# Optimization experiments

Hardware: AMD Instinct MI355X
Metric: run time of the kernel (lower is better)

The kernel has to match this reference:

```python
import jax, jax.numpy as jnp
import numpy as np

# static multi-scale pyramid (must match spatial_shapes array in setup_inputs)
SPATIAL = ((100, 100), (50, 50), (25, 25), (13, 13))
E, H, L, P = 256, 8, 4, 8   # embed_dims, num_heads, num_levels, num_points
BS, NQ = 2, 10000
LEN_VAL = sum(h * w for h, w in SPATIAL)


def _bilinear_gather(val, grid, Hs, Ws):
    """val: [BH, Hs*Ws, d]; grid: [BH, N, 2] in [-1,1].
    Matches F.grid_sample(mode='bilinear', padding_mode='zeros', align_corners=False)."""
    x = (grid[..., 0] + 1.0) * (Ws * 0.5) - 0.5
    y = (grid[..., 1] + 1.0) * (Hs * 0.5) - 0.5
    x0 = jnp.floor(x).astype(jnp.int32)
    y0 = jnp.floor(y).astype(jnp.int32)
    x1, y1 = x0 + 1, y0 + 1
    wx1 = x - x0.astype(x.dtype)
    wy1 = y - y0.astype(y.dtype)
    wx0, wy0 = 1.0 - wx1, 1.0 - wy1

    def corner(xi, yi, w):
        valid = (xi >= 0) & (xi < Ws) & (yi >= 0) & (yi < Hs)
        idx = jnp.clip(yi, 0, Hs - 1) * Ws + jnp.clip(xi, 0, Ws - 1)  # [BH, N]
        v = jnp.take_along_axis(val, idx[..., None], axis=1)          # [BH, N, d]
        return v * (w * valid.astype(w.dtype))[..., None]

    return (corner(x0, y0, wx0 * wy0) + corner(x1, y0, wx1 * wy0)
            + corner(x0, y1, wx0 * wy1) + corner(x1, y1, wx1 * wy1))


def setup_inputs() -> dict:
    key = jax.random.key(0)
    ks = jax.random.split(key, 10)
    scale = 1.0 / np.sqrt(E)
    inp = {
        'query': jax.random.normal(ks[0], (BS, NQ, E), jnp.float32),
        'value': jax.random.normal(ks[1], (BS, LEN_VAL, E), jnp.float32),
        'query_pos': 0.1 * jax.random.normal(ks[2], (BS, NQ, E), jnp.float32),
        'reference_points': jax.random.uniform(ks[3], (BS, NQ, L, 2), jnp.float32),
        'spatial_shapes': jnp.array(SPATIAL, dtype=jnp.int32),
        'W_off': 0.02 * jax.random.normal(ks[4], (E, H * L * P * 2), jnp.float32),
        'b_off': 0.5 * jax.random.normal(ks[5], (H * L * P * 2,), jnp.float32),
        'W_attn': 0.02 * jax.random.normal(ks[6], (E, H * L * P), jnp.float32),
        'b_attn': jnp.zeros((H * L * P,), jnp.float32),
        'W_val': scale * jax.random.normal(ks[7], (E, E), jnp.float32),
        'b_val': jnp.zeros((E,), jnp.float32),
        'W_out': scale * jax.random.normal(ks[8], (E, E), jnp.float32),
        'b_out': jnp.zeros((E,), jnp.float32),
    }
    return inp


def reference(query, value, query_pos, reference_points, spatial_shapes,
              W_off, b_off, W_attn, b_attn, W_val, b_val, W_out, b_out):
    d = E // H
    q = query + query_pos                                        # [bs, nq, E]
    bs, nq, _ = q.shape
    v = (value @ W_val + b_val).reshape(bs, LEN_VAL, H, d)       # [bs, len, H, d]
    off = (q @ W_off + b_off).reshape(bs, nq, H, L, P, 2)
    aw = jax.nn.softmax((q @ W_attn + b_attn).reshape(bs, nq, H, L * P), axis=-1)
    aw = aw.reshape(bs, nq, H, L, P)
    # normalizer is (W, H) per level
    norm = jnp.stack([spatial_shapes[:, 1], spatial_shapes[:, 0]], -1).astype(q.dtype)
    loc = reference_points[:, :, None, :, None, :] + off / norm[None, None, None, :, None, :]
    grids = 2.0 * loc - 1.0                                      # [bs, nq, H, L, P, 2]

    out = jnp.zeros((bs, nq, H, d), q.dtype)
    start = 0
    for lvl, (Hs, Ws) in enumerate(SPATIAL):
        v_l = v[:, start:start + Hs * Ws]                        # [bs, HW, H, d]
        start += Hs * Ws
        v_l = v_l.transpose(0, 2, 1, 3).reshape(bs * H, Hs * Ws, d)
        g_l = grids[:, :, :, lvl].transpose(0, 2, 1, 3, 4).reshape(bs * H, nq * P, 2)
        s = _bilinear_gather(v_l, g_l, Hs, Ws).reshape(bs, H, nq, P, d)
        w_l = aw[:, :, :, lvl].transpose(0, 2, 1, 3)             # [bs, H, nq, P]
        out = out + jnp.einsum('bhnpc,bhnp->bnhc', s, w_l)
    return out.reshape(bs, nq, E) @ W_out + b_out
```

## Files before the change

kernel.cpp:

```cpp
#include <hip/hip_runtime.h>


#define EE   256
#define HH   8
#define LL   4
#define NQq  10000
#define BSB  2
#define LENV 13294
#define MQ   16
#define ROWS_V (BSB * LENV)

#define VWS_OFF 393216

typedef unsigned short u16;
typedef unsigned int   u32;
typedef __attribute__((ext_vector_type(8))) short bf16x8;
typedef __attribute__((ext_vector_type(4))) float f32x4;

__device__ __forceinline__ u32 bf16_of(float f) {
  u32 u = __float_as_uint(f);
  return (u + 0x7FFFu + ((u >> 16) & 1u)) >> 16;
}
__device__ __forceinline__ float blo(u32 u) { return __uint_as_float(u << 16); }
__device__ __forceinline__ float bhi(u32 u) { return __uint_as_float(u & 0xFFFF0000u); }

__device__ __forceinline__ uint4 pack8(const float* f) {
  uint4 u;
  u.x = bf16_of(f[0]) | (bf16_of(f[1]) << 16);
  u.y = bf16_of(f[2]) | (bf16_of(f[3]) << 16);
  u.z = bf16_of(f[4]) | (bf16_of(f[5]) << 16);
  u.w = bf16_of(f[6]) | (bf16_of(f[7]) << 16);
  return u;
}

__device__ __forceinline__ void acc8(float o[8], uint4 q, float w) {
  o[0] += w * blo(q.x); o[1] += w * bhi(q.x);
  o[2] += w * blo(q.y); o[3] += w * bhi(q.y);
  o[4] += w * blo(q.z); o[5] += w * bhi(q.z);
  o[6] += w * blo(q.w); o[7] += w * bhi(q.w);
}

__global__ __launch_bounds__(64) void k_prep(
    const float* __restrict__ W_off, const float* __restrict__ W_attn,
    const float* __restrict__ W_val, const float* __restrict__ W_out,
    u16* __restrict__ wcat, u16* __restrict__ wval, u16* __restrict__ wout) {
  const int tile = blockIdx.x >> 3, s = blockIdx.x & 7;
  const int l = threadIdx.x, quad = l >> 4, r16 = l & 15;
  float f[8];
  u16* dst;
  if (tile < 48) {
    int col = tile * 16 + r16;
#pragma unroll
    for (int j = 0; j < 8; ++j) {
      int k = s * 32 + quad * 8 + j;
      f[j] = (col < 512) ? W_off[k * 512 + col] : W_attn[k * 256 + (col - 512)];
    }
    dst = wcat + ((tile * 8 + s) * 64 + l) * 8;
  } else if (tile < 64) {
    int col = (tile - 48) * 16 + r16;
#pragma unroll
    for (int j = 0; j < 8; ++j) f[j] = W_val[(s * 32 + quad * 8 + j) * 256 + col];
    dst = wval + (((tile - 48) * 8 + s) * 64 + l) * 8;
  } else {
    int col = (tile - 64) * 16 + r16;
#pragma unroll
    for (int j = 0; j < 8; ++j) f[j] = W_out[(s * 32 + quad * 8 + j) * 256 + col];
    dst = wout + (((tile - 64) * 8 + s) * 64 + l) * 8;
  }
  *(uint4*)dst = pack8(f);
}

__global__ __launch_bounds__(256) void k_valproj(
    const float* __restrict__ value, const float* __restrict__ b_val,
    const u16* __restrict__ wval, u16* __restrict__ v_ws) {
  __shared__ __align__(16) u16 sA[64][264];
  const int tid = threadIdx.x;
  const int g0 = blockIdx.x * 64;
#pragma unroll
  for (int ch = 0; ch < 8; ++ch) {
    int fidx = ch * 2048 + tid * 8;
    int row = fidx >> 8, col = fidx & 255;
    int g = g0 + row;
    float fv[8] = {0.f, 0.f, 0.f, 0.f, 0.f, 0.f, 0.f, 0.f};
    if (g < ROWS_V) {
      float4 a = *(const float4*)(value + (long)g * 256 + col);
      float4 b = *(const float4*)(value + (long)g * 256 + col + 4);
      fv[0] = a.x; fv[1] = a.y; fv[2] = a.z; fv[3] = a.w;
      fv[4] = b.x; fv[5] = b.y; fv[6] = b.z; fv[7] = b.w;
    }
    *(uint4*)&sA[row][col] = pack8(fv);
  }
  __syncthreads();
  const int wave = tid >> 6, lane = tid & 63, quad = lane >> 4, r16 = lane & 15;
  f32x4 acc[4][4] = {};
  for (int s = 0; s < 8; ++s) {
    bf16x8 af[4];
#pragma unroll
    for (int mt = 0; mt < 4; ++mt)
      af[mt] = *(const bf16x8*)&sA[mt * 16 + r16][s * 32 + quad * 8];
#pragma unroll
    for (int nt = 0; nt < 4; ++nt) {
      bf16x8 bfg = *(const bf16x8*)(wval + (((wave * 4 + nt) * 8 + s) * 64 + lane) * 8);
#pragma unroll
      for (int mt = 0; mt < 4; ++mt)
        acc[nt][mt] = __builtin_amdgcn_mfma_f32_16x16x32_bf16(af[mt], bfg, acc[nt][mt], 0, 0, 0);
    }
  }
  __syncthreads();
#pragma unroll
  for (int nt = 0; nt < 4; ++nt) {
    int col = (wave * 4 + nt) * 16 + r16;
    float bias = b_val[col];
#pragma unroll
    for (int mt = 0; mt < 4; ++mt)
#pragma unroll
      for (int rr = 0; rr < 4; ++rr)
        sA[mt * 16 + quad * 4 + rr][col] = (u16)bf16_of(acc[nt][mt][rr] + bias);
  }
  __syncthreads();
#pragma unroll
  for (int it = 0; it < 8; ++it) {
    int chunk = it * 256 + tid;
    int r  = chunk >> 5;
    int hc = chunk & 31;
    int h2 = hc >> 2, qq = hc & 3;
    int g = g0 + r;
    if (g < ROWS_V) {
      int bb = g / LENV, pix = g - bb * LENV;
      *(uint4*)(v_ws + ((long)((bb * 8 + h2) * LENV + pix) * 32 + qq * 8)) =
          *(const uint4*)&sA[r][h2 * 32 + qq * 8];
    }
  }
}

__global__ __launch_bounds__(512, 6) void k_attn(
    const float* __restrict__ query, const float* __restrict__ query_pos,
    const float* __restrict__ refpts,
    const float* __restrict__ b_off, const float* __restrict__ b_attn,
    const float* __restrict__ b_out,
    const u16* __restrict__ wcat, const u16* __restrict__ wout,
    const char* __restrict__ wsb, float* __restrict__ out) {
  __shared__ __align__(16) char smem[49408];
  u16   (*sQ)[264]   = (u16(*)[264])smem;
  float (*sC)[772]   = (float(*)[772])smem;
  uint2 (*sWgt)[256] = (uint2(*)[256])smem;
  u32   (*sOff)[256] = (u32(*)[256])(smem + 32768);
  u16   (*sO)[264]   = (u16(*)[264])smem;

  const int tid = threadIdx.x;
  const int g0 = blockIdx.x * MQ;
  const int b = g0 / NQq;
  const int q0 = g0 - b * NQq;
  const int wave = tid >> 6, lane = tid & 63, quad = lane >> 4, r16 = lane & 15;

  {
    int fidx = tid * 8;
    int row = fidx >> 8, col = fidx & 255;
    long base = ((long)(b * NQq + q0 + row)) * 256 + col;
    float4 a0 = *(const float4*)(query + base);
    float4 a1 = *(const float4*)(query + base + 4);
    float4 p0 = *(const float4*)(query_pos + base);
    float4 p1 = *(const float4*)(query_pos + base + 4);
    float fv[8] = {a0.x + p0.x, a0.y + p0.y, a0.z + p0.z, a0.w + p0.w,
                   a1.x + p1.x, a1.y + p1.y, a1.z + p1.z, a1.w + p1.w};
    *(uint4*)&sQ[row][col] = pack8(fv);
  }
  __syncthreads();

  f32x4 acc[6] = {};
  for (int s = 0; s < 8; ++s) {
    bf16x8 af = *(const bf16x8*)&sQ[r16][s * 32 + quad * 8];
#pragma unroll
    for (int t6 = 0; t6 < 6; ++t6) {
      int tile = wave * 6 + t6;
      bf16x8 bfg = *(const bf16x8*)(wcat + ((tile * 8 + s) * 64 + lane) * 8);
      acc[t6] = __builtin_amdgcn_mfma_f32_16x16x32_bf16(af, bfg, acc[t6], 0, 0, 0);
    }
  }
  __syncthreads();
#pragma unroll
  for (int t6 = 0; t6 < 6; ++t6) {
    int col = (wave * 6 + t6) * 16 + r16;
#pragma unroll
    for (int rr = 0; rr < 4; ++rr)
      sC[quad * 4 + rr][col] = acc[t6][rr];
  }
  __syncthreads();

  {
    const int m = tid >> 5, hh = (tid >> 2) & 7, g = tid & 3;
    float* p = &sC[m][512 + hh * 32 + g * 8];
    const float* ba = b_attn + hh * 32 + g * 8;
    float v[8];
    float mx = -1e30f;
#pragma unroll
    for (int j = 0; j < 8; ++j) { v[j] = p[j] + ba[j]; mx = fmaxf(mx, v[j]); }
    mx = fmaxf(mx, __shfl_xor(mx, 1));
    mx = fmaxf(mx, __shfl_xor(mx, 2));
    float sum = 0.f;
#pragma unroll
    for (int j = 0; j < 8; ++j) { v[j] = __expf(v[j] - mx); sum += v[j]; }
    sum += __shfl_xor(sum, 1);
    sum += __shfl_xor(sum, 2);
    float inv = 1.f / sum;
#pragma unroll
    for (int j = 0; j < 8; ++j) p[j] = v[j] * inv;
  }
  __syncthreads();

  uint2 wrecs[8];
  u32   orecs[8];
  {
    const int s = tid & 255, mh = tid >> 8;
    const int l = (s >> 3) & 3;
    const int WlI[4] = {100, 50, 25, 13};
    const int baseI[4] = {0, 10000, 12500, 13125};
    const int Wl = WlI[l], Hl = WlI[l], base = baseI[l];
    const float WlF = (float)Wl;
    const float box = b_off[2 * s], boy = b_off[2 * s + 1];
#pragma unroll
    for (int mm = 0; mm < 8; ++mm) {
      int m = mh * 8 + mm;
      float w = sC[m][512 + s];
      float ax = sC[m][2 * s], ay = sC[m][2 * s + 1];
      float2 rp = *(const float2*)(refpts + (((long)(b * NQq + q0 + m)) * LL + l) * 2);
      float x = rp.x * WlF + (ax + box) - 0.5f;
      float y = rp.y * WlF + (ay + boy) - 0.5f;
      float fx0 = floorf(x), fy0 = floorf(y);
      int x0 = (int)fx0, y0 = (int)fy0;
      float fx = x - fx0, fy = y - fy0;
      bool xv0 = (x0 >= 0) & (x0 < Wl);
      bool xv1 = (x0 >= -1) & (x0 < Wl - 1);
      bool yv0 = (y0 >= 0) & (y0 < Hl);
      bool yv1 = (y0 >= -1) & (y0 < Hl - 1);
      float w00 = w * (1.f - fx) * (1.f - fy) * (float)(xv0 & yv0);
      float w01 = w * fx * (1.f - fy) * (float)(xv1 & yv0);
      float w10 = w * (1.f - fx) * fy * (float)(xv0 & yv1);
      float w11 = w * fx * fy * (float)(xv1 & yv1);
      int x0a = min(max(x0, -1), Wl - 1);
      int y0a = min(max(y0, -1), Hl - 1);
      int y1c = min(max(y0 + 1, 0), Hl - 1);
      int o00u = base + y0a * Wl + x0a;
      u32 dyu  = (u32)((y1c - y0a) * Wl);
      wrecs[mm].x = bf16_of(w00) | (bf16_of(w01) << 16);
      wrecs[mm].y = bf16_of(w10) | (bf16_of(w11) << 16);
      orecs[mm]   = (u32)(o00u + 128) | (dyu << 14);
    }
  }
  __syncthreads();
  {
    const int s = tid & 255, mh = tid >> 8;
    const int jsw = (s & 224) | ((s + (s >> 5)) & 31);
#pragma unroll
    for (int mm = 0; mm < 8; ++mm) {
      sWgt[mh * 8 + mm][jsw] = wrecs[mm];
      sOff[mh * 8 + mm][jsw] = orecs[mm];
    }
  }
  __syncthreads();

  {
    const int c4 = tid & 3, hh = (tid >> 2) & 7, m = tid >> 5;
    const u32 vbm = (u32)VWS_OFF + (u32)(b * 8 + hh) * (u32)(LENV * 64)
                  + (u32)c4 * 16u - 8192u;
    float oacc[8] = {};
#pragma unroll 4
    for (int i = 0; i < 32; ++i) {
      const int srow = (hh << 5) | ((i + hh) & 31);
      uint2 wr = sWgt[m][srow];
      u32   po = sOff[m][srow];
      u32 off0 = vbm + ((po & 0x3FFFu) << 6);
      u32 off1 = off0 + ((po >> 14) << 6);
      uint4 q00 = *(const uint4*)(wsb + off0);
      uint4 q01 = *(const uint4*)(wsb + off0 + 64);
      uint4 q10 = *(const uint4*)(wsb + off1);
      uint4 q11 = *(const uint4*)(wsb + off1 + 64);
      float w00 = blo(wr.x), w01 = bhi(wr.x);
      float w10 = blo(wr.y), w11 = bhi(wr.y);
      acc8(oacc, q00, w00);
      acc8(oacc, q01, w01);
      acc8(oacc, q10, w10);
      acc8(oacc, q11, w11);
    }
    __syncthreads();
    *(uint4*)&sO[m][hh * 32 + c4 * 8] = pack8(oacc);
  }
  __syncthreads();

  f32x4 acc2[2] = {};
  for (int s = 0; s < 8; ++s) {
    bf16x8 af = *(const bf16x8*)&sO[r16][s * 32 + quad * 8];
#pragma unroll
    for (int t2 = 0; t2 < 2; ++t2) {
      int tile = wave * 2 + t2;
      bf16x8 bfg = *(const bf16x8*)(wout + ((tile * 8 + s) * 64 + lane) * 8);
      acc2[t2] = __builtin_amdgcn_mfma_f32_16x16x32_bf16(af, bfg, acc2[t2], 0, 0, 0);
    }
  }
#pragma unroll
  for (int t2 = 0; t2 < 2; ++t2) {
    int col = (wave * 2 + t2) * 16 + r16;
    float bias = b_out[col];
#pragma unroll
    for (int rr = 0; rr < 4; ++rr) {
      int row = quad * 4 + rr;
      out[((long)(b * NQq + q0 + row)) * 256 + col] = acc2[t2][rr] + bias;
    }
  }
}

extern "C" void kernel_launch(void* const* d_in, const int* in_sizes, int n_in,
                              void* d_out, int out_size, void* d_ws, size_t ws_size,
                              hipStream_t stream) {
  const float* query     = (const float*)d_in[0];
  const float* value     = (const float*)d_in[1];
  const float* query_pos = (const float*)d_in[2];
  const float* refpts    = (const float*)d_in[3];
  const float* W_off     = (const float*)d_in[5];
  const float* b_off     = (const float*)d_in[6];
  const float* W_attn    = (const float*)d_in[7];
  const float* b_attn    = (const float*)d_in[8];
  const float* W_val     = (const float*)d_in[9];
  const float* b_val     = (const float*)d_in[10];
  const float* W_out     = (const float*)d_in[11];
  const float* b_out     = (const float*)d_in[12];
  float* out = (float*)d_out;

  char* ws = (char*)d_ws;
  u16* wcat = (u16*)ws;
  u16* v_ws = (u16*)(ws + VWS_OFF);
  u16* wval = (u16*)(ws + VWS_OFF + 13613056);
  u16* wout = (u16*)(ws + VWS_OFF + 13613056 + 131072);

  k_prep<<<dim3(80 * 8), dim3(64), 0, stream>>>(W_off, W_attn, W_val, W_out,
                                                wcat, wval, wout);
  k_valproj<<<dim3((ROWS_V + 63) / 64), dim3(256), 0, stream>>>(value, b_val, wval, v_ws);
  k_attn<<<dim3(BSB * NQq / MQ), dim3(512), 0, stream>>>(
      query, query_pos, refpts, b_off, b_attn, b_out, wcat, wout, ws, out);
}
```

Baseline: 237.3 us.

## Split fused attention kernel into projection, head-major gather, and output stages

```diff
diff --git a/kernel.cpp b/kernel.cpp
--- a/kernel.cpp
+++ b/kernel.cpp
@@ -10,7 +10,11 @@
 #define MQ   16
 #define ROWS_V (BSB * LENV)
 
-#define VWS_OFF 393216
+#define VWS_OFF  393216
+#define GW_OFF   14268416
+#define GO_OFF   55228416
+#define GOUT_OFF 65468416
+#define WS_NEED  75708416
 
 typedef unsigned short u16;
 typedef unsigned int   u32;
@@ -70,15 +74,15 @@
   *(uint4*)dst = pack8(f);
 }
 
-__global__ __launch_bounds__(256) void k_valproj(
+__global__ __launch_bounds__(512) void k_valproj(
     const float* __restrict__ value, const float* __restrict__ b_val,
     const u16* __restrict__ wval, u16* __restrict__ v_ws) {
   __shared__ __align__(16) u16 sA[64][264];
   const int tid = threadIdx.x;
   const int g0 = blockIdx.x * 64;
 #pragma unroll
-  for (int ch = 0; ch < 8; ++ch) {
-    int fidx = ch * 2048 + tid * 8;
+  for (int ch = 0; ch < 4; ++ch) {
+    int fidx = ch * 4096 + tid * 8;
     int row = fidx >> 8, col = fidx & 255;
     int g = g0 + row;
     float fv[8] = {0.f, 0.f, 0.f, 0.f, 0.f, 0.f, 0.f, 0.f};
@@ -92,15 +96,16 @@
   }
   __syncthreads();
   const int wave = tid >> 6, lane = tid & 63, quad = lane >> 4, r16 = lane & 15;
-  f32x4 acc[4][4] = {};
+  f32x4 acc[2][4] = {};
   for (int s = 0; s < 8; ++s) {
     bf16x8 af[4];
 #pragma unroll
     for (int mt = 0; mt < 4; ++mt)
       af[mt] = *(const bf16x8*)&sA[mt * 16 + r16][s * 32 + quad * 8];
 #pragma unroll
-    for (int nt = 0; nt < 4; ++nt) {
-      bf16x8 bfg = *(const bf16x8*)(wval + (((wave * 4 + nt) * 8 + s) * 64 + lane) * 8);
+    for (int nt = 0; nt < 2; ++nt) {
+      int ntg = wave * 2 + nt;
+      bf16x8 bfg = *(const bf16x8*)(wval + ((ntg * 8 + s) * 64 + lane) * 8);
 #pragma unroll
       for (int mt = 0; mt < 4; ++mt)
         acc[nt][mt] = __builtin_amdgcn_mfma_f32_16x16x32_bf16(af[mt], bfg, acc[nt][mt], 0, 0, 0);
@@ -108,8 +113,8 @@
   }
   __syncthreads();
 #pragma unroll
-  for (int nt = 0; nt < 4; ++nt) {
-    int col = (wave * 4 + nt) * 16 + r16;
+  for (int nt = 0; nt < 2; ++nt) {
+    int col = (wave * 2 + nt) * 16 + r16;
     float bias = b_val[col];
 #pragma unroll
     for (int mt = 0; mt < 4; ++mt)
@@ -119,8 +124,8 @@
   }
   __syncthreads();
 #pragma unroll
-  for (int it = 0; it < 8; ++it) {
-    int chunk = it * 256 + tid;
+  for (int it = 0; it < 4; ++it) {
+    int chunk = it * 512 + tid;
     int r  = chunk >> 5;
     int hc = chunk & 31;
     int h2 = hc >> 2, qq = hc & 3;
@@ -133,7 +138,202 @@
   }
 }
 
-__global__ __launch_bounds__(512, 6) void k_attn(
+__global__ __launch_bounds__(512, 6) void k_attn_a(
+    const float* __restrict__ query, const float* __restrict__ query_pos,
+    const float* __restrict__ refpts,
+    const float* __restrict__ b_off, const float* __restrict__ b_attn,
+    const u16* __restrict__ wcat,
+    uint2* __restrict__ gW, u16* __restrict__ gO) {
+  __shared__ __align__(16) char smem[49408];
+  u16   (*sQ)[264] = (u16(*)[264])smem;
+  float (*sC)[772] = (float(*)[772])smem;
+
+  const int tid = threadIdx.x;
+  const int g0 = blockIdx.x * MQ;
+  const int b = g0 / NQq;
+  const int q0 = g0 - b * NQq;
+  const int wave = tid >> 6, lane = tid & 63, quad = lane >> 4, r16 = lane & 15;
+
+  {
+    int fidx = tid * 8;
+    int row = fidx >> 8, col = fidx & 255;
+    long base = ((long)(b * NQq + q0 + row)) * 256 + col;
+    float4 a0 = *(const float4*)(query + base);
+    float4 a1 = *(const float4*)(query + base + 4);
+    float4 p0 = *(const float4*)(query_pos + base);
+    float4 p1 = *(const float4*)(query_pos + base + 4);
+    float fv[8] = {a0.x + p0.x, a0.y + p0.y, a0.z + p0.z, a0.w + p0.w,
+                   a1.x + p1.x, a1.y + p1.y, a1.z + p1.z, a1.w + p1.w};
+    *(uint4*)&sQ[row][col] = pack8(fv);
+  }
+  __syncthreads();
+
+  f32x4 acc[6] = {};
+  for (int s = 0; s < 8; ++s) {
+    bf16x8 af = *(const bf16x8*)&sQ[r16][s * 32 + quad * 8];
+#pragma unroll
+    for (int t6 = 0; t6 < 6; ++t6) {
+      int tile = wave * 6 + t6;
+      bf16x8 bfg = *(const bf16x8*)(wcat + ((tile * 8 + s) * 64 + lane) * 8);
+      acc[t6] = __builtin_amdgcn_mfma_f32_16x16x32_bf16(af, bfg, acc[t6], 0, 0, 0);
+    }
+  }
+  __syncthreads();
+#pragma unroll
+  for (int t6 = 0; t6 < 6; ++t6) {
+    int col = (wave * 6 + t6) * 16 + r16;
+#pragma unroll
+    for (int rr = 0; rr < 4; ++rr)
+      sC[quad * 4 + rr][col] = acc[t6][rr];
+  }
+  __syncthreads();
+
+  {
+    const int m = tid >> 5, hh = (tid >> 2) & 7, g = tid & 3;
+    float* p = &sC[m][512 + hh * 32 + g * 8];
+    const float* ba = b_attn + hh * 32 + g * 8;
+    float v[8];
+    float mx = -1e30f;
+#pragma unroll
+    for (int j = 0; j < 8; ++j) { v[j] = p[j] + ba[j]; mx = fmaxf(mx, v[j]); }
+    mx = fmaxf(mx, __shfl_xor(mx, 1));
+    mx = fmaxf(mx, __shfl_xor(mx, 2));
+    float sum = 0.f;
+#pragma unroll
+    for (int j = 0; j < 8; ++j) { v[j] = __expf(v[j] - mx); sum += v[j]; }
+    sum += __shfl_xor(sum, 1);
+    sum += __shfl_xor(sum, 2);
+    float inv = 1.f / sum;
+#pragma unroll
+    for (int j = 0; j < 8; ++j) p[j] = v[j] * inv;
+  }
+  __syncthreads();
+
+  {
+    const int s = tid & 255, mh = tid >> 8;
+    const int l = (s >> 3) & 3;
+    const int WlI[4] = {100, 50, 25, 13};
+    const int baseI[4] = {0, 10000, 12500, 13125};
+    const int Wl = WlI[l], Hl = WlI[l], base = baseI[l];
+    const float WlF = (float)Wl;
+    const float box = b_off[2 * s], boy = b_off[2 * s + 1];
+    const long rb = ((long)(b * NQq + q0 + mh * 8)) * 256 + s;
+#pragma unroll
+    for (int mm = 0; mm < 8; ++mm) {
+      int m = mh * 8 + mm;
+      float w = sC[m][512 + s];
+      float ax = sC[m][2 * s], ay = sC[m][2 * s + 1];
+      float2 rp = *(const float2*)(refpts + (((long)(b * NQq + q0 + m)) * LL + l) * 2);
+      float x = rp.x * WlF + (ax + box) - 0.5f;
+      float y = rp.y * WlF + (ay + boy) - 0.5f;
+      float fx0 = floorf(x), fy0 = floorf(y);
+      int x0 = (int)fx0, y0 = (int)fy0;
+      float fx = x - fx0, fy = y - fy0;
+      bool xv0 = (x0 >= 0) & (x0 < Wl);
+      bool xv1 = (x0 >= -1) & (x0 < Wl - 1);
+      bool yv0 = (y0 >= 0) & (y0 < Hl);
+      bool yv1 = (y0 >= -1) & (y0 < Hl - 1);
+      float w00 = w * (1.f - fx) * (1.f - fy) * (float)(xv0 & yv0);
+      float w01 = w * fx * (1.f - fy) * (float)(xv1 & yv0);
+      float w10 = w * (1.f - fx) * fy * (float)(xv0 & yv1);
+      float w11 = w * fx * fy * (float)(xv1 & yv1);
+      int x0a = min(max(x0, -1), Wl - 1);
+      int y0a = min(max(y0, -1), Hl - 1);
+      int y1c = min(max(y0 + 1, 0), Hl - 1);
+      int o00u = base + y0a * Wl + x0a;
+      int dyf  = y1c - y0a;
+      uint2 wr;
+      wr.x = bf16_of(w00) | (bf16_of(w01) << 16);
+      wr.y = bf16_of(w10) | (bf16_of(w11) << 16);
+      gW[rb + mm * 256] = wr;
+      gO[rb + mm * 256] = (u16)((o00u + 128) | (dyf << 14));
+    }
+  }
+}
+
+__global__ __launch_bounds__(512, 6) void k_gather(
+    const uint2* __restrict__ gW, const u16* __restrict__ gO,
+    const char* __restrict__ wsb, u16* __restrict__ gOut) {
+  const int h = blockIdx.x & 7;
+  const int t = blockIdx.x >> 3;
+  const int b = t & 1;
+  const int chunk = t >> 1;
+  const int c4 = threadIdx.x & 3;
+  const int ql = threadIdx.x >> 2;
+  const int q = chunk * 128 + ql;
+  if (q >= NQq) return;
+  const long rbase = ((long)(b * NQq + q)) * 256 + h * 32;
+  const u32 vbm = (u32)VWS_OFF + (u32)(b * 8 + h) * (u32)(LENV * 64)
+                + (u32)c4 * 16u - 8192u;
+  float oacc[8] = {};
+#pragma unroll
+  for (int g = 0; g < 4; ++g) {
+    const u32 WL64 = (u32)(g == 0 ? 100 : g == 1 ? 50 : g == 2 ? 25 : 13) * 64u;
+    const uint2* wp = gW + rbase + g * 8;
+    uint4 wb0 = *(const uint4*)(wp);
+    uint4 wb1 = *(const uint4*)(wp + 2);
+    uint4 wb2 = *(const uint4*)(wp + 4);
+    uint4 wb3 = *(const uint4*)(wp + 6);
+    uint4 ob  = *(const uint4*)(gO + rbase + g * 8);
+    u32 offs[8] = {ob.x & 0xFFFFu, ob.x >> 16, ob.y & 0xFFFFu, ob.y >> 16,
+                   ob.z & 0xFFFFu, ob.z >> 16, ob.w & 0xFFFFu, ob.w >> 16};
+    u32 wx[8] = {wb0.x, wb0.z, wb1.x, wb1.z, wb2.x, wb2.z, wb3.x, wb3.z};
+    u32 wy[8] = {wb0.y, wb0.w, wb1.y, wb1.w, wb2.y, wb2.w, wb3.y, wb3.w};
+#pragma unroll
+    for (int j = 0; j < 8; ++j) {
+      u32 o0 = vbm + ((offs[j] & 0x3FFFu) << 6);
+      u32 o1 = o0 + (offs[j] >> 14) * WL64;
+      uint4 q00 = *(const uint4*)(wsb + o0);
+      uint4 q01 = *(const uint4*)(wsb + o0 + 64);
+      uint4 q10 = *(const uint4*)(wsb + o1);
+      uint4 q11 = *(const uint4*)(wsb + o1 + 64);
+      acc8(oacc, q00, blo(wx[j]));
+      acc8(oacc, q01, bhi(wx[j]));
+      acc8(oacc, q10, blo(wy[j]));
+      acc8(oacc, q11, bhi(wy[j]));
+    }
+  }
+  *(uint4*)(gOut + rbase + c4 * 8) = pack8(oacc);
+}
+
+__global__ __launch_bounds__(512) void k_out(
+    const u16* __restrict__ gOut, const u16* __restrict__ wout,
+    const float* __restrict__ b_out, float* __restrict__ out) {
+  __shared__ __align__(16) u16 sO[16][264];
+  const int tid = threadIdx.x;
+  const int g0 = blockIdx.x * MQ;
+  const int b = g0 / NQq;
+  const int q0 = g0 - b * NQq;
+  const int wave = tid >> 6, lane = tid & 63, quad = lane >> 4, r16 = lane & 15;
+  {
+    int row = tid >> 5, col = (tid * 8) & 255;
+    *(uint4*)&sO[row][col] =
+        *(const uint4*)(gOut + ((long)(b * NQq + q0 + row)) * 256 + col);
+  }
+  __syncthreads();
+  f32x4 acc2[2] = {};
+  for (int s = 0; s < 8; ++s) {
+    bf16x8 af = *(const bf16x8*)&sO[r16][s * 32 + quad * 8];
+#pragma unroll
+    for (int t2 = 0; t2 < 2; ++t2) {
+      int tile = wave * 2 + t2;
+      bf16x8 bfg = *(const bf16x8*)(wout + ((tile * 8 + s) * 64 + lane) * 8);
+      acc2[t2] = __builtin_amdgcn_mfma_f32_16x16x32_bf16(af, bfg, acc2[t2], 0, 0, 0);
+    }
+  }
+#pragma unroll
+  for (int t2 = 0; t2 < 2; ++t2) {
+    int col = (wave * 2 + t2) * 16 + r16;
+    float bias = b_out[col];
+#pragma unroll
+    for (int rr = 0; rr < 4; ++rr) {
+      int row = quad * 4 + rr;
+      out[((long)(b * NQq + q0 + row)) * 256 + col] = acc2[t2][rr] + bias;
+    }
+  }
+}
+
+__global__ __launch_bounds__(512, 6) void k_attn_fused(
     const float* __restrict__ query, const float* __restrict__ query_pos,
     const float* __restrict__ refpts,
     const float* __restrict__ b_off, const float* __restrict__ b_attn,
@@ -275,12 +475,10 @@
       uint4 q01 = *(const uint4*)(wsb + off0 + 64);
       uint4 q10 = *(const uint4*)(wsb + off1);
       uint4 q11 = *(const uint4*)(wsb + off1 + 64);
-      float w00 = blo(wr.x), w01 = bhi(wr.x);
-      float w10 = blo(wr.y), w11 = bhi(wr.y);
-      acc8(oacc, q00, w00);
-      acc8(oacc, q01, w01);
-      acc8(oacc, q10, w10);
-      acc8(oacc, q11, w11);
+      acc8(oacc, q00, blo(wr.x));
+      acc8(oacc, q01, bhi(wr.x));
+      acc8(oacc, q10, blo(wr.y));
+      acc8(oacc, q11, bhi(wr.y));
     }
     __syncthreads();
     *(uint4*)&sO[m][hh * 32 + c4 * 8] = pack8(oacc);
@@ -334,7 +532,19 @@
 
   k_prep<<<dim3(80 * 8), dim3(64), 0, stream>>>(W_off, W_attn, W_val, W_out,
                                                 wcat, wval, wout);
-  k_valproj<<<dim3((ROWS_V + 63) / 64), dim3(256), 0, stream>>>(value, b_val, wval, v_ws);
-  k_attn<<<dim3(BSB * NQq / MQ), dim3(512), 0, stream>>>(
-      query, query_pos, refpts, b_off, b_attn, b_out, wcat, wout, ws, out);
-}
+  k_valproj<<<dim3((ROWS_V + 63) / 64), dim3(512), 0, stream>>>(value, b_val, wval, v_ws);
+
+  if (ws_size >= (size_t)WS_NEED) {
+    uint2* gW  = (uint2*)(ws + GW_OFF);
+    u16*  gO   = (u16*)(ws + GO_OFF);
+    u16*  gOut = (u16*)(ws + GOUT_OFF);
+    k_attn_a<<<dim3(BSB * NQq / MQ), dim3(512), 0, stream>>>(
+        query, query_pos, refpts, b_off, b_attn, wcat, gW, gO);
+    k_gather<<<dim3(((NQq + 127) / 128) * BSB * HH), dim3(512), 0, stream>>>(
+        gW, gO, ws, gOut);
+    k_out<<<dim3(BSB * NQq / MQ), dim3(512), 0, stream>>>(gOut, wout, b_out, out);
+  } else {
+    k_attn_fused<<<dim3(BSB * NQq / MQ), dim3(512), 0, stream>>>(
+        query, query_pos, refpts, b_off, b_attn, b_out, wcat, wout, ws, out);
+  }
+}
```

Result: slower. 254.2 us (+7.1%).
